# Performance work log

Measured on AMD Instinct MI355X. Metric: run time of the kernel, lower is better.

The kernel has to match this reference:

```python
import jax, jax.numpy as jnp
import numpy as np

H = 64  # hidden_size
B, S, DIN = 256, 4096, 1
NUM_LAYERS = 3


def setup_inputs() -> dict:
    key = jax.random.key(0)
    ks = jax.random.split(key, 32)
    s = 1.0 / np.sqrt(H)  # torch LSTM/Linear init bound
    inp = {"x": jax.random.normal(ks[0], (B, S, DIN), dtype=jnp.float32)}
    ki = 1
    for l in range(NUM_LAYERS):
        din = DIN if l == 0 else H
        inp[f"Wih{l}"] = jax.random.uniform(ks[ki], (4 * H, din), minval=-s, maxval=s); ki += 1
        inp[f"Whh{l}"] = jax.random.uniform(ks[ki], (4 * H, H), minval=-s, maxval=s); ki += 1
        inp[f"bih{l}"] = jax.random.uniform(ks[ki], (4 * H,), minval=-s, maxval=s); ki += 1
        inp[f"bhh{l}"] = jax.random.uniform(ks[ki], (4 * H,), minval=-s, maxval=s); ki += 1
    inp["Wlin"] = jax.random.uniform(ks[ki], (1, H), minval=-s, maxval=s); ki += 1
    inp["blin"] = jax.random.uniform(ks[ki], (1,), minval=-s, maxval=s)
    return inp


def _lstm_layer(x, Wih, Whh, bih, bhh):
    """x: [B,S,Din] -> (hs [B,S,H], h_T [B,H], c_T [B,H]). PyTorch gate order i,f,g,o."""
    # precompute input contribution for all timesteps (one big GEMM)
    xg = jnp.einsum('bsd,gd->bsg', x, Wih) + (bih + bhh)  # [B,S,4H]
    b = x.shape[0]
    h0 = jnp.zeros((b, H), x.dtype)
    c0 = jnp.zeros((b, H), x.dtype)

    def step(carry, xg_t):
        h, c = carry
        g = xg_t + h @ Whh.T  # [B,4H]
        i, f, gg, o = jnp.split(g, 4, axis=-1)
        c = jax.nn.sigmoid(f) * c + jax.nn.sigmoid(i) * jnp.tanh(gg)
        h = jax.nn.sigmoid(o) * jnp.tanh(c)
        return (h, c), h

    (hT, cT), hs = jax.lax.scan(step, (h0, c0), jnp.swapaxes(xg, 0, 1))
    return jnp.swapaxes(hs, 0, 1), hT, cT


def reference(x, Wih0, Whh0, bih0, bhh0, Wih1, Whh1, bih1, bhh1,
              Wih2, Whh2, bih2, bhh2, Wlin, blin):
    layers = [(Wih0, Whh0, bih0, bhh0), (Wih1, Whh1, bih1, bhh1), (Wih2, Whh2, bih2, bhh2)]
    out = x
    hTs, cTs = [], []
    for (Wih, Whh, bih, bhh) in layers:
        out, hT, cT = _lstm_layer(out, Wih, Whh, bih, bhh)
        hTs.append(hT); cTs.append(cT)
    y = out @ Wlin.T + blin  # [B,S,1]
    h_n = jnp.stack(hTs, axis=0)  # [num_layers,B,H]
    c_n = jnp.stack(cTs, axis=0)
    return y, h_n, c_n
```

## Files before the change

kernel.cpp:

```cpp
#include <hip/hip_runtime.h>
#include <stdint.h>


#define SQ 4096
#define HH 64
#define NB 256

typedef _Float16 h2    __attribute__((ext_vector_type(2)));
typedef _Float16 f16x8 __attribute__((ext_vector_type(8)));
typedef float    f32x4 __attribute__((ext_vector_type(4)));

__device__ __forceinline__ float frcp(float x)  { return __builtin_amdgcn_rcpf(x); }
__device__ __forceinline__ float fexp2(float x) { return __builtin_amdgcn_exp2f(x); }

__device__ __forceinline__ void pin4(uint4& r) {
    asm volatile("" : "+v"(r.x), "+v"(r.y), "+v"(r.z), "+v"(r.w));
}
__device__ __forceinline__ void pinv(f32x4& r) {
    float t0 = r[0], t1 = r[1], t2 = r[2], t3 = r[3];
    asm volatile("" : "+v"(t0), "+v"(t1), "+v"(t2), "+v"(t3));
    r[0] = t0; r[1] = t1; r[2] = t2; r[3] = t3;
}

__device__ __forceinline__ f32x4 mm(uint4 hv, uint4 wv, f32x4 c) {
    return __builtin_amdgcn_mfma_f32_16x16x32_f16(
        __builtin_bit_cast(f16x8, hv), __builtin_bit_cast(f16x8, wv), c, 0, 0, 0);
}

__global__ __launch_bounds__(256)
void prep_weights(const float* __restrict__ Whh0, const float* __restrict__ Wih1,
                  const float* __restrict__ Whh1, const float* __restrict__ Wih2,
                  const float* __restrict__ Whh2, const float* __restrict__ Wlin,
                  uint32_t* __restrict__ ws)
{
    const int idx = blockIdx.x * 256 + threadIdx.x;
    if (idx >= 40960) {
        const int r  = idx - 40960;
        const int jj = r & 3;
        const int l  = (r >> 2) & 63;
        const int kk = (r >> 8) & 1;
        const int n  = l & 15;
        const int krow = ((l >> 4) << 3) + 2 * jj;
        const int ku   = 32 * kk + krow;
        h2 t;
        t[0] = (_Float16)((n == 0) ? Wlin[ku]     : 0.f);
        t[1] = (_Float16)((n == 0) ? Wlin[ku + 1] : 0.f);
        ws[idx] = __builtin_bit_cast(uint32_t, t);
        return;
    }
    int r, ktbits;
    const float *Wi = nullptr, *Wh;
    if (idx < 8192)       { r = idx;         ktbits = 1; Wh = Whh0; }
    else if (idx < 24576) { r = idx - 8192;  ktbits = 2; Wi = Wih1; Wh = Whh1; }
    else                  { r = idx - 24576; ktbits = 2; Wi = Wih2; Wh = Whh2; }
    const int jj  = r & 3;
    const int l   = (r >> 2) & 63;
    const int rem = r >> 8;
    const int kt  = rem & ((1 << ktbits) - 1);
    const int tw  = rem >> ktbits;
    const int j   = tw & 3;
    const int w   = tw >> 2;
    const int n   = l & 15;
    const int krow = ((l >> 4) << 3) + 2 * jj;
    const int orow = 64 * j + 16 * w + n;
    int kcol = 32 * kt + krow;
    const float* M;
    if (ktbits == 1)    { M = Wh; }
    else if (kcol < 64) { M = Wi; }
    else                { M = Wh; kcol -= 64; }
    h2 t;
    t[0] = (_Float16)M[orow * HH + kcol];
    t[1] = (_Float16)M[orow * HH + kcol + 1];
    ws[idx] = __builtin_bit_cast(uint32_t, t);
}

__global__ __launch_bounds__(768)
__attribute__((amdgpu_waves_per_eu(3)))
void lstm3_fused(
    const float* __restrict__ x,
    const float* __restrict__ Wih0,
    const float* __restrict__ bih0, const float* __restrict__ bhh0,
    const float* __restrict__ bih1, const float* __restrict__ bhh1,
    const float* __restrict__ bih2, const float* __restrict__ bhh2,
    const float* __restrict__ blin,
    const uint32_t* __restrict__ wpk,
    float* __restrict__ out)
{
    const int b    = blockIdx.x;
    const int tid  = threadIdx.x;
    const int grp  = tid >> 8;
    const int k    = tid & 255;
    const int w    = k >> 6;
    const int l    = k & 63;
    const int n    = l & 15;
    const int q    = l >> 4;
    const int unit = 16 * w + n;
    const bool grp0w1 = (grp == 0) && (w == 1);

    __shared__ __align__(16) float xrow[SQ + 8];
    __shared__ __align__(16) uint4 hbf[2][3][8];
    __shared__ __align__(16) float ystage[32];

    for (int i = tid; i < SQ; i += 768) xrow[i] = x[b * SQ + i];
    if (tid < 8) xrow[SQ + tid] = 0.f;
    if (tid < 48) ((uint4*)hbf)[tid] = make_uint4(0, 0, 0, 0);

    const int gbase = (grp == 0) ? 0 : (grp == 1) ? 8192 : 24576;
    const int KT    = (grp == 0) ? 2 : 4;
    const uint32_t* wbp = wpk + gbase;
    auto fr = [&](int j_, int kt_) {
        return *reinterpret_cast<const uint4*>(
            wbp + (((w * 4 + j_) * KT + kt_) * 64 + l) * 4);
    };
    uint4 w00 = fr(0, 0), w01 = fr(0, 1), w10 = fr(1, 0), w11 = fr(1, 1),
          w20 = fr(2, 0), w21 = fr(2, 1), w30 = fr(3, 0), w31 = fr(3, 1);
    pin4(w00); pin4(w01); pin4(w10); pin4(w11);
    pin4(w20); pin4(w21); pin4(w30); pin4(w31);
    uint4 w02 = {}, w03 = {}, w12 = {}, w13 = {},
          w22 = {}, w23 = {}, w32 = {}, w33 = {};
    if (grp != 0) {
        w02 = fr(0, 2); w03 = fr(0, 3); w12 = fr(1, 2); w13 = fr(1, 3);
        w22 = fr(2, 2); w23 = fr(2, 3); w32 = fr(3, 2); w33 = fr(3, 3);
        pin4(w02); pin4(w03); pin4(w12); pin4(w13);
        pin4(w22); pin4(w23); pin4(w32); pin4(w33);
    }
    uint4 wy2 = {}, wy3 = {};
    f32x4 cy = {0.f, 0.f, 0.f, 0.f};
    if (grp0w1) {
        wy2 = *reinterpret_cast<const uint4*>(wpk + 40960 + (0 * 64 + l) * 4);
        wy3 = *reinterpret_cast<const uint4*>(wpk + 40960 + (1 * 64 + l) * 4);
        pin4(wy2); pin4(wy3);
        const float bv = blin[0];
        cy = f32x4{bv, bv, bv, bv};
        pinv(cy);
    }

    const float* bi = (grp == 0) ? bih0 : (grp == 1) ? bih1 : bih2;
    const float* bh = (grp == 0) ? bhh0 : (grp == 1) ? bhh1 : bhh2;
    const float bs0 = bi[unit]       + bh[unit];
    const float bs1 = bi[64 + unit]  + bh[64 + unit];
    const float bs2 = bi[128 + unit] + bh[128 + unit];
    const float bs3 = bi[192 + unit] + bh[192 + unit];
    f32x4 cb0 = {bs0, bs0, bs0, bs0};  pinv(cb0);
    f32x4 cb1 = {bs1, bs1, bs1, bs1};  pinv(cb1);
    f32x4 cb2 = {bs2, bs2, bs2, bs2};  pinv(cb2);
    f32x4 cb3 = {bs3, bs3, bs3, bs3};  pinv(cb3);

    float wx0 = 0.f, wx1 = 0.f, wx2 = 0.f, wx3 = 0.f;
    if (grp == 0) {
        wx0 = Wih0[unit];       wx1 = Wih0[64 + unit];
        wx2 = Wih0[128 + unit]; wx3 = Wih0[192 + unit];
    }

    const int la = (grp == 2) ? 1 : 0;
    const int lb = grp;
    const uint4* pA[2] = { &hbf[0][la][q], &hbf[1][la][q] };
    const uint4* pB[2] = { &hbf[0][lb][q], &hbf[1][lb][q] };
    const uint4* pY[2] = { &hbf[0][2][q],  &hbf[1][2][q] };
    _Float16* pH[2] = { (_Float16*)&hbf[0][grp][0] + unit,
                        (_Float16*)&hbf[1][grp][0] + unit };

    float cc = 0.f;
    f32x4 ai0 = cb0, ai1 = cb1, ai2 = cb2, ai3 = cb3;

    __syncthreads();

    auto tick = [&](int T, int rd) {
        const int wr = rd ^ 1;
        float xT = 0.f;
        if (grp == 0) xT = xrow[T];

        f32x4 d0, d1, d2, d3;
        const uint4 a0 = pA[rd][0], a1 = pA[rd][4];
        if (grp == 0) {
            d0 = mm(a0, w00, cb0);  d1 = mm(a0, w10, cb1);
            d2 = mm(a0, w20, cb2);  d3 = mm(a0, w30, cb3);
            d0 = mm(a1, w01, d0);   d1 = mm(a1, w11, d1);
            d2 = mm(a1, w21, d2);   d3 = mm(a1, w31, d3);
        } else {
            const uint4 c0 = pB[rd][0], c1 = pB[rd][4];
            d0 = mm(c0, w02, ai0);  d1 = mm(c0, w12, ai1);
            d2 = mm(c0, w22, ai2);  d3 = mm(c0, w32, ai3);
            d0 = mm(c1, w03, d0);   d1 = mm(c1, w13, d1);
            d2 = mm(c1, w23, d2);   d3 = mm(c1, w33, d3);
            ai0 = mm(a0, w00, cb0); ai1 = mm(a0, w10, cb1);
            ai2 = mm(a0, w20, cb2); ai3 = mm(a0, w30, cb3);
            ai0 = mm(a1, w01, ai0); ai1 = mm(a1, w11, ai1);
            ai2 = mm(a1, w21, ai2); ai3 = mm(a1, w31, ai3);
        }

        if (grp0w1) {
            const int sy = T - 5;
            if (sy >= 0 && sy < SQ) {
                const uint4 y0 = pY[rd][0], y1 = pY[rd][4];
                f32x4 d4 = mm(y0, wy2, cy);
                d4 = mm(y1, wy3, d4);
                if (l == 0) ystage[sy & 31] = d4[0];
                if ((sy & 31) == 31) {
                    const float yv = ystage[l & 31];
                    if (l < 32) out[b * SQ + (sy - 31) + l] = yv;
                }
            }
        }

        const int step = T - 2 * grp;
        if (step >= 0 && step < SQ) {
            float gi = d0[0], gf = d1[0], gg = d2[0], go = d3[0];
            if (grp == 0) {
                gi += wx0 * xT; gf += wx1 * xT;
                gg += wx2 * xT; go += wx3 * xT;
            }
            const float i_ = frcp(1.f + fexp2(gi * -1.44269504f));
            const float f_ = frcp(1.f + fexp2(gf * -1.44269504f));
            const float o_ = frcp(1.f + fexp2(go * -1.44269504f));
            const float tg = 2.f * frcp(1.f + fexp2(gg * -2.88539008f)) - 1.f;
            cc = f_ * cc + i_ * tg;
            const float tc = fminf(fmaxf(cc, -15.f), 15.f);
            const float e  = fexp2(tc * -2.88539008f);
            const float h  = o_ * ((1.f - e) * frcp(1.f + e));
            if (l < 16) {
                pH[wr][0] = (_Float16)h;
                if (step == SQ - 1) {
                    out[NB * SQ + grp * NB * HH + b * HH + unit] = h;
                    out[NB * SQ + 3 * NB * HH + grp * NB * HH + b * HH + unit] = cc;
                }
            }
        }
        __syncthreads();
    };

    for (int T = 0; T < SQ + 6; T += 2) {
        tick(T, 0);
        tick(T + 1, 1);
    }
}

extern "C" void kernel_launch(void* const* d_in, const int* in_sizes, int n_in,
                              void* d_out, int out_size, void* d_ws, size_t ws_size,
                              hipStream_t stream) {
    const float* x    = (const float*)d_in[0];
    const float* Wih0 = (const float*)d_in[1];
    const float* Whh0 = (const float*)d_in[2];
    const float* bih0 = (const float*)d_in[3];
    const float* bhh0 = (const float*)d_in[4];
    const float* Wih1 = (const float*)d_in[5];
    const float* Whh1 = (const float*)d_in[6];
    const float* bih1 = (const float*)d_in[7];
    const float* bhh1 = (const float*)d_in[8];
    const float* Wih2 = (const float*)d_in[9];
    const float* Whh2 = (const float*)d_in[10];
    const float* bih2 = (const float*)d_in[11];
    const float* bhh2 = (const float*)d_in[12];
    const float* Wlin = (const float*)d_in[13];
    const float* blin = (const float*)d_in[14];
    float* out = (float*)d_out;

    uint32_t* wpk = (uint32_t*)d_ws;
    prep_weights<<<162, 256, 0, stream>>>(Whh0, Wih1, Whh1, Wih2, Whh2, Wlin, wpk);
    lstm3_fused<<<NB, 768, 0, stream>>>(x, Wih0, bih0, bhh0,
                                        bih1, bhh1, bih2, bhh2,
                                        blin, wpk, out);
}
```

Before: 2.626 ms.

## Split LSTM layers into separate blocks linked by global-memory flag rings

```diff
diff --git a/kernel.cpp b/kernel.cpp
--- a/kernel.cpp
+++ b/kernel.cpp
@@ -5,6 +5,15 @@
 #define SQ 4096
 #define HH 64
 #define NB 256
+#define SPIN 2048
+
+#define WOFF_FLAG0 41472
+#define WOFF_FLAG1 41728
+#define WOFF_CONS1 41984
+#define WOFF_CONS2 42240
+#define WOFF_RING0 65536
+#define WOFF_RING1 327680
+#define WS_U32_TOTAL 589824
 
 typedef _Float16 h2    __attribute__((ext_vector_type(2)));
 typedef _Float16 f16x8 __attribute__((ext_vector_type(8)));
@@ -20,6 +29,13 @@
     float t0 = r[0], t1 = r[1], t2 = r[2], t3 = r[3];
     asm volatile("" : "+v"(t0), "+v"(t1), "+v"(t2), "+v"(t3));
     r[0] = t0; r[1] = t1; r[2] = t2; r[3] = t3;
+}
+
+__device__ __forceinline__ uint32_t fldu(const uint32_t* p) {
+    return __hip_atomic_load(p, __ATOMIC_RELAXED, __HIP_MEMORY_SCOPE_AGENT);
+}
+__device__ __forceinline__ void fstu(uint32_t* p, uint32_t v) {
+    __hip_atomic_store(p, v, __ATOMIC_RELAXED, __HIP_MEMORY_SCOPE_AGENT);
 }
 
 __device__ __forceinline__ f32x4 mm(uint4 hv, uint4 wv, f32x4 c) {
@@ -34,6 +50,7 @@
                   uint32_t* __restrict__ ws)
 {
     const int idx = blockIdx.x * 256 + threadIdx.x;
+    if (idx >= 41472) { ws[idx] = 0; return; }
     if (idx >= 40960) {
         const int r  = idx - 40960;
         const int jj = r & 3;
@@ -74,7 +91,211 @@
     ws[idx] = __builtin_bit_cast(uint32_t, t);
 }
 
-__global__ __launch_bounds__(768)
+template<int ROLE>
+__device__ __forceinline__ void run_block(
+    int b, int tid,
+    const uint32_t* __restrict__ wpk, uint32_t* __restrict__ wsu,
+    const float* __restrict__ Wih0,
+    const float* __restrict__ bi, const float* __restrict__ bh,
+    const float* __restrict__ blin,
+    float* __restrict__ out,
+    float* xrow, uint4 (*hbf)[8], float* ystage)
+{
+    const int w    = tid >> 6;
+    const int l    = tid & 63;
+    const int n    = l & 15;
+    const int q    = l >> 4;
+    const int unit = 16 * w + n;
+    constexpr int KT = (ROLE == 0) ? 2 : 4;
+    constexpr int GB = (ROLE == 0) ? 0 : (ROLE == 1) ? 8192 : 24576;
+
+    auto fr = [&](int j_, int kt_) {
+        return *reinterpret_cast<const uint4*>(
+            wpk + GB + (((w * 4 + j_) * KT + kt_) * 64 + l) * 4);
+    };
+    uint4 w00 = fr(0, 0), w01 = fr(0, 1), w10 = fr(1, 0), w11 = fr(1, 1),
+          w20 = fr(2, 0), w21 = fr(2, 1), w30 = fr(3, 0), w31 = fr(3, 1);
+    pin4(w00); pin4(w01); pin4(w10); pin4(w11);
+    pin4(w20); pin4(w21); pin4(w30); pin4(w31);
+    uint4 w02 = {}, w03 = {}, w12 = {}, w13 = {},
+          w22 = {}, w23 = {}, w32 = {}, w33 = {};
+    if constexpr (ROLE != 0) {
+        w02 = fr(0, 2); w03 = fr(0, 3); w12 = fr(1, 2); w13 = fr(1, 3);
+        w22 = fr(2, 2); w23 = fr(2, 3); w32 = fr(3, 2); w33 = fr(3, 3);
+        pin4(w02); pin4(w03); pin4(w12); pin4(w13);
+        pin4(w22); pin4(w23); pin4(w32); pin4(w33);
+    }
+    uint4 wy2 = {}, wy3 = {};
+    f32x4 cy = {0.f, 0.f, 0.f, 0.f};
+    if constexpr (ROLE == 2) {
+        if (w == 0) {
+            wy2 = *reinterpret_cast<const uint4*>(wpk + 40960 + (0 * 64 + l) * 4);
+            wy3 = *reinterpret_cast<const uint4*>(wpk + 40960 + (1 * 64 + l) * 4);
+            pin4(wy2); pin4(wy3);
+            const float bv = blin[0];
+            cy = f32x4{bv, bv, bv, bv};
+            pinv(cy);
+        }
+    }
+
+    const float bs0 = bi[unit]       + bh[unit];
+    const float bs1 = bi[64 + unit]  + bh[64 + unit];
+    const float bs2 = bi[128 + unit] + bh[128 + unit];
+    const float bs3 = bi[192 + unit] + bh[192 + unit];
+    f32x4 cb0 = {bs0, bs0, bs0, bs0};  pinv(cb0);
+    f32x4 cb1 = {bs1, bs1, bs1, bs1};  pinv(cb1);
+    f32x4 cb2 = {bs2, bs2, bs2, bs2};  pinv(cb2);
+    f32x4 cb3 = {bs3, bs3, bs3, bs3};  pinv(cb3);
+
+    float wx0 = 0.f, wx1 = 0.f, wx2 = 0.f, wx3 = 0.f;
+    if constexpr (ROLE == 0) {
+        wx0 = Wih0[unit];       wx1 = Wih0[64 + unit];
+        wx2 = Wih0[128 + unit]; wx3 = Wih0[192 + unit];
+    }
+
+    uint32_t* Fprod = wsu + ((ROLE == 0) ? WOFF_FLAG0 : WOFF_FLAG1) + b;
+    uint32_t* Fin   = wsu + ((ROLE == 1) ? WOFF_FLAG0 : WOFF_FLAG1) + b;
+    uint32_t* Cin   = wsu + ((ROLE == 0) ? WOFF_CONS1 : WOFF_CONS2) + b;
+    uint32_t* Cself = wsu + ((ROLE == 1) ? WOFF_CONS1 : WOFF_CONS2) + b;
+    uint32_t* ringP = wsu + ((ROLE == 0) ? WOFF_RING0 : WOFF_RING1) + b * 1024;
+    uint32_t* ringI = wsu + ((ROLE == 1) ? WOFF_RING0 : WOFF_RING1) + b * 1024;
+
+    uint4 ha0 = {}, ha1 = {};
+    uint32_t flagv = 0;
+    int have = -1;
+    float cc = 0.f;
+
+    for (int s = 0; s < SQ; ++s) {
+        const int rd = s & 1, wr = rd ^ 1;
+
+        if constexpr (ROLE != 2) {
+            if (w == 0) {
+                if ((s & 7) == 0 && s >= 32) {
+                    const uint32_t need = (uint32_t)(s - 25);
+                    for (int it = 0; it < SPIN; ++it)
+                        if (fldu(Cin) >= need) break;
+                }
+                asm volatile("s_waitcnt vmcnt(0)" ::: "memory");
+                if (l == 0 && s >= 2) fstu(Fprod, (uint32_t)(s - 1));
+                if (s >= 1 && l < 32) {
+                    const uint32_t hw = ((const uint32_t*)&hbf[rd])[l];
+                    fstu(ringP + ((s - 1) & 31) * 32 + l, hw);
+                }
+            }
+        }
+
+        if constexpr (ROLE != 0) {
+            if (have < s) {
+                for (int it = 0; it < SPIN; ++it) {
+                    flagv = fldu(Fin);
+                    if (flagv >= (uint32_t)(s + 1)) break;
+                }
+                const uint32_t* bse = ringI + (s & 31) * 32;
+                ha0 = uint4{fldu(bse + q * 4),     fldu(bse + q * 4 + 1),
+                            fldu(bse + q * 4 + 2), fldu(bse + q * 4 + 3)};
+                ha1 = uint4{fldu(bse + 16 + q * 4),     fldu(bse + 16 + q * 4 + 1),
+                            fldu(bse + 16 + q * 4 + 2), fldu(bse + 16 + q * 4 + 3)};
+                have = s;
+            }
+        }
+
+        const uint4 c0 = hbf[rd][q], c1 = hbf[rd][4 + q];
+        f32x4 d0, d1, d2, d3;
+        if constexpr (ROLE == 0) {
+            d0 = mm(c0, w00, cb0);  d1 = mm(c0, w10, cb1);
+            d2 = mm(c0, w20, cb2);  d3 = mm(c0, w30, cb3);
+            d0 = mm(c1, w01, d0);   d1 = mm(c1, w11, d1);
+            d2 = mm(c1, w21, d2);   d3 = mm(c1, w31, d3);
+        } else {
+            d0 = mm(ha0, w00, cb0); d1 = mm(ha0, w10, cb1);
+            d2 = mm(ha0, w20, cb2); d3 = mm(ha0, w30, cb3);
+            d0 = mm(ha1, w01, d0);  d1 = mm(ha1, w11, d1);
+            d2 = mm(ha1, w21, d2);  d3 = mm(ha1, w31, d3);
+            d0 = mm(c0, w02, d0);   d1 = mm(c0, w12, d1);
+            d2 = mm(c0, w22, d2);   d3 = mm(c0, w32, d3);
+            d0 = mm(c1, w03, d0);   d1 = mm(c1, w13, d1);
+            d2 = mm(c1, w23, d2);   d3 = mm(c1, w33, d3);
+        }
+
+        if constexpr (ROLE == 2) {
+            if (w == 0) {
+                const int sy = s - 1;
+                if (sy >= 0) {
+                    f32x4 d4 = mm(c0, wy2, cy);
+                    d4 = mm(c1, wy3, d4);
+                    if (l == 0) ystage[sy & 31] = d4[0];
+                    if ((sy & 31) == 31) {
+                        const float yv = ystage[l & 31];
+                        if (l < 32) out[b * SQ + (sy - 31) + l] = yv;
+                    }
+                }
+            }
+        }
+
+        if constexpr (ROLE != 0) {
+            const uint32_t fnew = fldu(Fin);
+            if (flagv >= (uint32_t)(s + 2) && have == s && s + 1 < SQ) {
+                const uint32_t* bse = ringI + ((s + 1) & 31) * 32;
+                ha0 = uint4{fldu(bse + q * 4),     fldu(bse + q * 4 + 1),
+                            fldu(bse + q * 4 + 2), fldu(bse + q * 4 + 3)};
+                ha1 = uint4{fldu(bse + 16 + q * 4),     fldu(bse + 16 + q * 4 + 1),
+                            fldu(bse + 16 + q * 4 + 2), fldu(bse + 16 + q * 4 + 3)};
+                have = s + 1;
+            }
+            if (fnew > flagv) flagv = fnew;
+            if ((s & 7) == 7 && tid == 0) fstu(Cself, (uint32_t)(s + 1));
+        }
+
+        float gi = d0[0], gf = d1[0], gg = d2[0], go = d3[0];
+        if constexpr (ROLE == 0) {
+            const float xT = xrow[s];
+            gi += wx0 * xT; gf += wx1 * xT;
+            gg += wx2 * xT; go += wx3 * xT;
+        }
+        const float i_ = frcp(1.f + fexp2(gi * -1.44269504f));
+        const float f_ = frcp(1.f + fexp2(gf * -1.44269504f));
+        const float o_ = frcp(1.f + fexp2(go * -1.44269504f));
+        const float tg = 2.f * frcp(1.f + fexp2(gg * -2.88539008f)) - 1.f;
+        cc = f_ * cc + i_ * tg;
+        const float tc = fminf(fmaxf(cc, -15.f), 15.f);
+        const float e  = fexp2(tc * -2.88539008f);
+        const float h  = o_ * ((1.f - e) * frcp(1.f + e));
+        if (l < 16) {
+            ((_Float16*)&hbf[wr])[unit] = (_Float16)h;
+            if (s == SQ - 1) {
+                out[NB * SQ + ROLE * NB * HH + b * HH + unit] = h;
+                out[NB * SQ + 3 * NB * HH + ROLE * NB * HH + b * HH + unit] = cc;
+            }
+        }
+
+        asm volatile("s_waitcnt lgkmcnt(0)" ::: "memory");
+        __builtin_amdgcn_s_barrier();
+        asm volatile("" ::: "memory");
+    }
+
+    if constexpr (ROLE != 2) {
+        if (w == 0) {
+            if (l < 32) {
+                const uint32_t hw = ((const uint32_t*)&hbf[SQ & 1])[l];
+                fstu(ringP + ((SQ - 1) & 31) * 32 + l, hw);
+            }
+            asm volatile("s_waitcnt vmcnt(0)" ::: "memory");
+            if (l == 0) fstu(Fprod, (uint32_t)SQ);
+        }
+    }
+    if constexpr (ROLE == 2) {
+        if (w == 0) {
+            const uint4 t0 = hbf[SQ & 1][q], t1 = hbf[SQ & 1][4 + q];
+            f32x4 d4 = mm(t0, wy2, cy);
+            d4 = mm(t1, wy3, d4);
+            if (l == 0) ystage[31] = d4[0];
+            const float yv = ystage[l & 31];
+            if (l < 32) out[b * SQ + (SQ - 32) + l] = yv;
+        }
+    }
+}
+
+__global__ __launch_bounds__(256)
 __attribute__((amdgpu_waves_per_eu(3)))
 void lstm3_fused(
     const float* __restrict__ x,
@@ -83,156 +304,28 @@
     const float* __restrict__ bih1, const float* __restrict__ bhh1,
     const float* __restrict__ bih2, const float* __restrict__ bhh2,
     const float* __restrict__ blin,
-    const uint32_t* __restrict__ wpk,
+    const uint32_t* __restrict__ wpk, uint32_t* __restrict__ wsu,
     float* __restrict__ out)
 {
-    const int b    = blockIdx.x;
+    const int role = blockIdx.x >> 8;
+    const int b    = blockIdx.x & 255;
     const int tid  = threadIdx.x;
-    const int grp  = tid >> 8;
-    const int k    = tid & 255;
-    const int w    = k >> 6;
-    const int l    = k & 63;
-    const int n    = l & 15;
-    const int q    = l >> 4;
-    const int unit = 16 * w + n;
-    const bool grp0w1 = (grp == 0) && (w == 1);
-
-    __shared__ __align__(16) float xrow[SQ + 8];
-    __shared__ __align__(16) uint4 hbf[2][3][8];
+
+    __shared__ __align__(16) float xrow[SQ];
+    __shared__ __align__(16) uint4 hbf[2][8];
     __shared__ __align__(16) float ystage[32];
 
-    for (int i = tid; i < SQ; i += 768) xrow[i] = x[b * SQ + i];
-    if (tid < 8) xrow[SQ + tid] = 0.f;
-    if (tid < 48) ((uint4*)hbf)[tid] = make_uint4(0, 0, 0, 0);
-
-    const int gbase = (grp == 0) ? 0 : (grp == 1) ? 8192 : 24576;
-    const int KT    = (grp == 0) ? 2 : 4;
-    const uint32_t* wbp = wpk + gbase;
-    auto fr = [&](int j_, int kt_) {
-        return *reinterpret_cast<const uint4*>(
-            wbp + (((w * 4 + j_) * KT + kt_) * 64 + l) * 4);
-    };
-    uint4 w00 = fr(0, 0), w01 = fr(0, 1), w10 = fr(1, 0), w11 = fr(1, 1),
-          w20 = fr(2, 0), w21 = fr(2, 1), w30 = fr(3, 0), w31 = fr(3, 1);
-    pin4(w00); pin4(w01); pin4(w10); pin4(w11);
-    pin4(w20); pin4(w21); pin4(w30); pin4(w31);
-    uint4 w02 = {}, w03 = {}, w12 = {}, w13 = {},
-          w22 = {}, w23 = {}, w32 = {}, w33 = {};
-    if (grp != 0) {
-        w02 = fr(0, 2); w03 = fr(0, 3); w12 = fr(1, 2); w13 = fr(1, 3);
-        w22 = fr(2, 2); w23 = fr(2, 3); w32 = fr(3, 2); w33 = fr(3, 3);
-        pin4(w02); pin4(w03); pin4(w12); pin4(w13);
-        pin4(w22); pin4(w23); pin4(w32); pin4(w33);
-    }
-    uint4 wy2 = {}, wy3 = {};
-    f32x4 cy = {0.f, 0.f, 0.f, 0.f};
-    if (grp0w1) {
-        wy2 = *reinterpret_cast<const uint4*>(wpk + 40960 + (0 * 64 + l) * 4);
-        wy3 = *reinterpret_cast<const uint4*>(wpk + 40960 + (1 * 64 + l) * 4);
-        pin4(wy2); pin4(wy3);
-        const float bv = blin[0];
-        cy = f32x4{bv, bv, bv, bv};
-        pinv(cy);
-    }
-
-    const float* bi = (grp == 0) ? bih0 : (grp == 1) ? bih1 : bih2;
-    const float* bh = (grp == 0) ? bhh0 : (grp == 1) ? bhh1 : bhh2;
-    const float bs0 = bi[unit]       + bh[unit];
-    const float bs1 = bi[64 + unit]  + bh[64 + unit];
-    const float bs2 = bi[128 + unit] + bh[128 + unit];
-    const float bs3 = bi[192 + unit] + bh[192 + unit];
-    f32x4 cb0 = {bs0, bs0, bs0, bs0};  pinv(cb0);
-    f32x4 cb1 = {bs1, bs1, bs1, bs1};  pinv(cb1);
-    f32x4 cb2 = {bs2, bs2, bs2, bs2};  pinv(cb2);
-    f32x4 cb3 = {bs3, bs3, bs3, bs3};  pinv(cb3);
-
-    float wx0 = 0.f, wx1 = 0.f, wx2 = 0.f, wx3 = 0.f;
-    if (grp == 0) {
-        wx0 = Wih0[unit];       wx1 = Wih0[64 + unit];
-        wx2 = Wih0[128 + unit]; wx3 = Wih0[192 + unit];
-    }
-
-    const int la = (grp == 2) ? 1 : 0;
-    const int lb = grp;
-    const uint4* pA[2] = { &hbf[0][la][q], &hbf[1][la][q] };
-    const uint4* pB[2] = { &hbf[0][lb][q], &hbf[1][lb][q] };
-    const uint4* pY[2] = { &hbf[0][2][q],  &hbf[1][2][q] };
-    _Float16* pH[2] = { (_Float16*)&hbf[0][grp][0] + unit,
-                        (_Float16*)&hbf[1][grp][0] + unit };
-
-    float cc = 0.f;
-    f32x4 ai0 = cb0, ai1 = cb1, ai2 = cb2, ai3 = cb3;
-
+    if (role == 0)
+        for (int i = tid; i < SQ; i += 256) xrow[i] = x[b * SQ + i];
+    if (tid < 16) ((uint4*)hbf)[tid] = make_uint4(0, 0, 0, 0);
     __syncthreads();
 
-    auto tick = [&](int T, int rd) {
-        const int wr = rd ^ 1;
-        float xT = 0.f;
-        if (grp == 0) xT = xrow[T];
-
-        f32x4 d0, d1, d2, d3;
-        const uint4 a0 = pA[rd][0], a1 = pA[rd][4];
-        if (grp == 0) {
-            d0 = mm(a0, w00, cb0);  d1 = mm(a0, w10, cb1);
-            d2 = mm(a0, w20, cb2);  d3 = mm(a0, w30, cb3);
-            d0 = mm(a1, w01, d0);   d1 = mm(a1, w11, d1);
-            d2 = mm(a1, w21, d2);   d3 = mm(a1, w31, d3);
-        } else {
-            const uint4 c0 = pB[rd][0], c1 = pB[rd][4];
-            d0 = mm(c0, w02, ai0);  d1 = mm(c0, w12, ai1);
-            d2 = mm(c0, w22, ai2);  d3 = mm(c0, w32, ai3);
-            d0 = mm(c1, w03, d0);   d1 = mm(c1, w13, d1);
-            d2 = mm(c1, w23, d2);   d3 = mm(c1, w33, d3);
-            ai0 = mm(a0, w00, cb0); ai1 = mm(a0, w10, cb1);
-            ai2 = mm(a0, w20, cb2); ai3 = mm(a0, w30, cb3);
-            ai0 = mm(a1, w01, ai0); ai1 = mm(a1, w11, ai1);
-            ai2 = mm(a1, w21, ai2); ai3 = mm(a1, w31, ai3);
-        }
-
-        if (grp0w1) {
-            const int sy = T - 5;
-            if (sy >= 0 && sy < SQ) {
-                const uint4 y0 = pY[rd][0], y1 = pY[rd][4];
-                f32x4 d4 = mm(y0, wy2, cy);
-                d4 = mm(y1, wy3, d4);
-                if (l == 0) ystage[sy & 31] = d4[0];
-                if ((sy & 31) == 31) {
-                    const float yv = ystage[l & 31];
-                    if (l < 32) out[b * SQ + (sy - 31) + l] = yv;
-                }
-            }
-        }
-
-        const int step = T - 2 * grp;
-        if (step >= 0 && step < SQ) {
-            float gi = d0[0], gf = d1[0], gg = d2[0], go = d3[0];
-            if (grp == 0) {
-                gi += wx0 * xT; gf += wx1 * xT;
-                gg += wx2 * xT; go += wx3 * xT;
-            }
-            const float i_ = frcp(1.f + fexp2(gi * -1.44269504f));
-            const float f_ = frcp(1.f + fexp2(gf * -1.44269504f));
-            const float o_ = frcp(1.f + fexp2(go * -1.44269504f));
-            const float tg = 2.f * frcp(1.f + fexp2(gg * -2.88539008f)) - 1.f;
-            cc = f_ * cc + i_ * tg;
-            const float tc = fminf(fmaxf(cc, -15.f), 15.f);
-            const float e  = fexp2(tc * -2.88539008f);
-            const float h  = o_ * ((1.f - e) * frcp(1.f + e));
-            if (l < 16) {
-                pH[wr][0] = (_Float16)h;
-                if (step == SQ - 1) {
-                    out[NB * SQ + grp * NB * HH + b * HH + unit] = h;
-                    out[NB * SQ + 3 * NB * HH + grp * NB * HH + b * HH + unit] = cc;
-                }
-            }
-        }
-        __syncthreads();
-    };
-
-    for (int T = 0; T < SQ + 6; T += 2) {
-        tick(T, 0);
-        tick(T + 1, 1);
-    }
+    if (role == 0)
+        run_block<0>(b, tid, wpk, wsu, Wih0, bih0, bhh0, blin, out, xrow, hbf, ystage);
+    else if (role == 1)
+        run_block<1>(b, tid, wpk, wsu, Wih0, bih1, bhh1, blin, out, xrow, hbf, ystage);
+    else
+        run_block<2>(b, tid, wpk, wsu, Wih0, bih2, bhh2, blin, out, xrow, hbf, ystage);
 }
 
 extern "C" void kernel_launch(void* const* d_in, const int* in_sizes, int n_in,
@@ -256,8 +349,8 @@
     float* out = (float*)d_out;
 
     uint32_t* wpk = (uint32_t*)d_ws;
-    prep_weights<<<162, 256, 0, stream>>>(Whh0, Wih1, Whh1, Wih2, Whh2, Wlin, wpk);
-    lstm3_fused<<<NB, 768, 0, stream>>>(x, Wih0, bih0, bhh0,
-                                        bih1, bhh1, bih2, bhh2,
-                                        blin, wpk, out);
-}
+    prep_weights<<<166, 256, 0, stream>>>(Whh0, Wih1, Whh1, Wih2, Whh2, Wlin, wpk);
+    lstm3_fused<<<768, 256, 0, stream>>>(x, Wih0, bih0, bhh0,
+                                         bih1, bhh1, bih2, bhh2,
+                                         blin, wpk, wpk, out);
+}
```

Result: slower. 10.47 ms (+298.9%).
